# Kernel tuning notes

Measured on AMD Instinct MI355X. Metric: run time of the kernel, lower is better.

Reference implementation:

```python
import jax, jax.numpy as jnp
import numpy as np

H = 64  # hidden size
I = 300  # input size
NEG_SLOPE = 0.01  # LeakyReLU default


def _gru_scan(x_proj, W_hh, b_hh):
    """x_proj: [T, B, 3H] precomputed input projections (+ b_ih).
    Returns all hidden states [T, B, H] starting from h0 = 0."""
    B = x_proj.shape[1]
    h0 = jnp.zeros((B, H), dtype=x_proj.dtype)

    def step(h, xp):
        gh = h @ W_hh.T + b_hh  # [B, 3H]
        xr, xz, xn = jnp.split(xp, 3, axis=-1)
        hr, hz, hn = jnp.split(gh, 3, axis=-1)
        r = jax.nn.sigmoid(xr + hr)
        z = jax.nn.sigmoid(xz + hz)
        n = jnp.tanh(xn + r * hn)
        h_new = (1.0 - z) * n + z * h
        return h_new, h_new

    _, hs = jax.lax.scan(step, h0, x_proj)
    return hs  # [T, B, H]


def _forward(x, W_ih_f, W_hh_f, b_ih_f, b_hh_f, W_ih_b, W_hh_b, b_ih_b, b_hh_b,
             W1, b1, W2, b2):
    # x: [B, T, I]
    xt = jnp.swapaxes(x, 0, 1)  # [T, B, I]
    xp_f = jnp.einsum('tbi,gi->tbg', xt, W_ih_f) + b_ih_f  # [T, B, 3H]
    xp_b = jnp.einsum('tbi,gi->tbg', xt[::-1], W_ih_b) + b_ih_b

    hs_f = _gru_scan(xp_f, W_hh_f, b_hh_f)            # [T, B, H]
    hs_b = _gru_scan(xp_b, W_hh_b, b_hh_b)[::-1]      # [T, B, H] (realigned)

    out = jnp.concatenate([hs_f, hs_b], axis=-1)      # [T, B, 2H]
    x_first = out[0]    # [B, 2H]
    x_last = out[-1]    # [B, 2H]
    feat = jnp.concatenate([x_first, x_last], axis=1)  # [B, 4H]

    h1 = feat @ W1.T + b1
    h1 = jnp.where(h1 >= 0, h1, NEG_SLOPE * h1)  # LeakyReLU
    return h1 @ W2.T + b2  # [B, 1]


def setup_inputs() -> dict:
    key = jax.random.key(0)
    ks = jax.random.split(key, 16)
    B, T = 256, 512
    s_gru = 1.0 / np.sqrt(H)
    s1 = 1.0 / np.sqrt(256)
    s2 = 1.0 / np.sqrt(32)
    u = lambda k, shape, s: jax.random.uniform(k, shape, jnp.float32, -s, s)
    return {
        'x': jax.random.normal(ks[0], (B, T, I), dtype=jnp.float32),
        'W_ih_f': u(ks[1], (3 * H, I), s_gru),
        'W_hh_f': u(ks[2], (3 * H, H), s_gru),
        'b_ih_f': u(ks[3], (3 * H,), s_gru),
        'b_hh_f': u(ks[4], (3 * H,), s_gru),
        'W_ih_b': u(ks[5], (3 * H, I), s_gru),
        'W_hh_b': u(ks[6], (3 * H, H), s_gru),
        'b_ih_b': u(ks[7], (3 * H,), s_gru),
        'b_hh_b': u(ks[8], (3 * H,), s_gru),
        'W1': u(ks[9], (32, 4 * H), s1),
        'b1': u(ks[10], (32,), s1),
        'W2': u(ks[11], (1, 32), s2),
        'b2': u(ks[12], (1,), s2),
    }


def reference(x, W_ih_f, W_hh_f, b_ih_f, b_hh_f, W_ih_b, W_hh_b, b_ih_b, b_hh_b,
              W1, b1, W2, b2):
    return _forward(x, W_ih_f, W_hh_f, b_ih_f, b_hh_f,
                    W_ih_b, W_hh_b, b_ih_b, b_hh_b, W1, b1, W2, b2)
```

## Files before the change

### kernel.cpp

```cpp
#include <hip/hip_runtime.h>
#include <hip/hip_bf16.h>
#include <math.h>

#define T_LEN 512
#define B_SZ  256
#define I_SZ  300
#define H_SZ  64
#define G3    192
#define TPG   3072
#define HPAD  80

typedef float    f4v __attribute__((ext_vector_type(4)));
typedef _Float16 h4v __attribute__((ext_vector_type(4)));
typedef _Float16 h8v __attribute__((ext_vector_type(8)));

__device__ __forceinline__ float sigm_f(float x) {
    return __builtin_amdgcn_rcpf(1.f + __expf(-x));
}
__device__ __forceinline__ float tanh_f(float x) {
    float a = fabsf(x);
    float e = __expf(2.f * a);
    float t = 1.f - 2.f * __builtin_amdgcn_rcpf(1.f + e);
    return copysignf(t, x);
}

__device__ __forceinline__ void lds_barrier() {
    __builtin_amdgcn_sched_barrier(0);
    asm volatile("s_waitcnt lgkmcnt(0)\n\ts_barrier" ::: "memory");
    __builtin_amdgcn_sched_barrier(0);
}

#define KC  64
#define NKC 5

__device__ __forceinline__ int stage_off(int j, int srow, int skq) {
    int g2 = (skq >> 1) & 3;
    return j * 1024 + (skq >> 3) * 512 + g2 * 128 + ((srow ^ (g2 << 1)) << 3) + (skq & 1) * 4;
}
__device__ __forceinline__ int frag_off(int tile, int kh, int lane) {
    int kgrp = lane >> 4, fr = lane & 15;
    return tile * 1024 + kh * 512 + kgrp * 128 + (((fr ^ (kgrp << 1))) << 3);
}

__global__ __launch_bounds__(256, 2) void proj_gemm(
    const float* __restrict__ x,
    const float* __restrict__ Wf, const float* __restrict__ bf,
    const float* __restrict__ Wb, const float* __restrict__ bb,
    _Float16* __restrict__ xp)
{
    __shared__ _Float16 Ap[8 * 1024];
    __shared__ _Float16 Bp[12 * 1024];

    const int tid = threadIdx.x;
    const int bid = blockIdx.x;
    const int d   = bid >> 10;
    const int G   = (bid >> 6) & 15;
    const int tc  = bid & 63;

    const float* W    = d ? Wb : Wf;
    const float* bias = d ? bb : bf;

    const int srow = tid >> 4;
    const int skq  = tid & 15;

    const int lane = tid & 63;
    const int w    = tid >> 6;

    f4v acc[2][12];
    #pragma unroll
    for (int t2 = 0; t2 < 2; ++t2)
        #pragma unroll
        for (int gt = 0; gt < 12; ++gt) acc[t2][gt] = (f4v)0.f;

    float4 av[8], bv[12];
    {
        const bool valid = (skq * 4) <= 296;
        #pragma unroll
        for (int j = 0; j < 8; ++j)
            av[j] = valid ? *(const float4*)(x + ((size_t)(G * 16 + srow) * T_LEN + tc * 8 + j) * I_SZ + skq * 4)
                          : float4{0.f, 0.f, 0.f, 0.f};
        #pragma unroll
        for (int j = 0; j < 12; ++j)
            bv[j] = valid ? *(const float4*)(W + (size_t)(j * 16 + srow) * I_SZ + skq * 4)
                          : float4{0.f, 0.f, 0.f, 0.f};
    }

    for (int kc = 0; kc < NKC; ++kc) {
        __syncthreads();

        #pragma unroll
        for (int j = 0; j < 8; ++j) {
            h4v c = { (_Float16)av[j].x, (_Float16)av[j].y,
                      (_Float16)av[j].z, (_Float16)av[j].w };
            *(h4v*)&Ap[stage_off(j, srow, skq)] = c;
        }
        #pragma unroll
        for (int j = 0; j < 12; ++j) {
            h4v c = { (_Float16)bv[j].x, (_Float16)bv[j].y,
                      (_Float16)bv[j].z, (_Float16)bv[j].w };
            *(h4v*)&Bp[stage_off(j, srow, skq)] = c;
        }
        __syncthreads();

        if (kc + 1 < NKC) {
            const int k0 = (kc + 1) * KC;
            const bool valid = (k0 + skq * 4) <= 296;
            #pragma unroll
            for (int j = 0; j < 8; ++j)
                av[j] = valid ? *(const float4*)(x + ((size_t)(G * 16 + srow) * T_LEN + tc * 8 + j) * I_SZ + k0 + skq * 4)
                              : float4{0.f, 0.f, 0.f, 0.f};
            #pragma unroll
            for (int j = 0; j < 12; ++j)
                bv[j] = valid ? *(const float4*)(W + (size_t)(j * 16 + srow) * I_SZ + k0 + skq * 4)
                              : float4{0.f, 0.f, 0.f, 0.f};
        }

        #pragma unroll
        for (int kh = 0; kh < 2; ++kh) {
            h8v xb0 = *(const h8v*)&Ap[frag_off(w * 2 + 0, kh, lane)];
            h8v xb1 = *(const h8v*)&Ap[frag_off(w * 2 + 1, kh, lane)];
            #pragma unroll
            for (int gt = 0; gt < 12; ++gt) {
                h8v wf = *(const h8v*)&Bp[frag_off(gt, kh, lane)];
                acc[0][gt] = __builtin_amdgcn_mfma_f32_16x16x32_f16(wf, xb0, acc[0][gt], 0, 0, 0);
                acc[1][gt] = __builtin_amdgcn_mfma_f32_16x16x32_f16(wf, xb1, acc[1][gt], 0, 0, 0);
            }
        }
    }

    const int col  = lane & 15;
    const int rowq = lane >> 4;
    _Float16* obase = xp + (size_t)(d * 16 + G) * T_LEN * TPG;
    #pragma unroll
    for (int t2 = 0; t2 < 2; ++t2) {
        int t = tc * 8 + w * 2 + t2;
        _Float16* ot = obase + (size_t)t * TPG;
        #pragma unroll
        for (int gt = 0; gt < 12; ++gt) {
            float4 bv4 = *(const float4*)(bias + gt * 16 + rowq * 4);
            h4v c = { (_Float16)(acc[t2][gt][0] + bv4.x),
                      (_Float16)(acc[t2][gt][1] + bv4.y),
                      (_Float16)(acc[t2][gt][2] + bv4.z),
                      (_Float16)(acc[t2][gt][3] + bv4.w) };
            *(h4v*)(ot + col * G3 + gt * 16 + rowq * 4) = c;
        }
    }
}

__global__ __launch_bounds__(256) void gru_scan(
    const _Float16* __restrict__ xp2,
    const float* __restrict__ Whf, const float* __restrict__ bhf,
    const float* __restrict__ Whb, const float* __restrict__ bhb,
    float* __restrict__ feat)
{
    const int tid  = threadIdx.x;
    const int lane = tid & 63;
    const int w    = tid >> 6;
    const int blk  = blockIdx.x;
    const int d    = blk >> 6;
    const int G    = (blk >> 2) & 15;
    const int sub  = blk & 3;
    const int col  = lane & 15;
    const int quad = lane >> 4;
    const int u    = w * 16 + col;
    const int bm   = sub * 4 + quad;

    const float* Whh = d ? Whb : Whf;
    const float* bhh = d ? bhb : bhf;

    h8v wb[3][2];
    f4v accb[3];
    int loff[3];
    #pragma unroll
    for (int g = 0; g < 3; ++g) {
        const int n = g * 64 + u;
        const float* wrow = Whh + (size_t)n * 64;
        #pragma unroll
        for (int c = 0; c < 2; ++c) {
            float4 w0 = *(const float4*)(wrow + c * 32 + quad * 8);
            float4 w1 = *(const float4*)(wrow + c * 32 + quad * 8 + 4);
            wb[g][c] = h8v{(_Float16)w0.x, (_Float16)w0.y, (_Float16)w0.z, (_Float16)w0.w,
                           (_Float16)w1.x, (_Float16)w1.y, (_Float16)w1.z, (_Float16)w1.w};
        }
        float bn = bhh[n];
        accb[g] = f4v{bn, bn, bn, bn};
        loff[g] = bm * G3 + n;
    }

    __shared__ _Float16 hs[2][4 * HPAD];
    for (int i = tid; i < 4 * HPAD; i += 256) hs[0][i] = (_Float16)0.f;
    float hold = 0.f;

    const long tstep = d ? -(long)TPG : (long)TPG;
    const _Float16* base = xp2 + (size_t)(d * 16 + G) * T_LEN * TPG
                               + (size_t)(d ? T_LEN - 1 : 0) * TPG;

    _Float16 px[2][3];
    #pragma unroll
    for (int g = 0; g < 3; ++g) {
        px[0][g] = base[loff[g]];
        px[1][g] = base[tstep + loff[g]];
    }
    const _Float16* pnext = base + 2 * tstep;

    const int off_first = d ? 192 : 0;
    const int off_last  = d ? 64 : 128;

    __syncthreads();

    for (int s = 0; s < T_LEN; s += 2) {
        #pragma unroll
        for (int j = 0; j < 2; ++j) {
            const int sj = s + j;
            const _Float16* hrd = hs[j];
            _Float16*       hwr = hs[j ^ 1];

            h8v a0 = *(const h8v*)&hrd[(col >> 2) * HPAD + quad * 8];
            h8v a1 = *(const h8v*)&hrd[(col >> 2) * HPAD + 32 + quad * 8];

            f4v gh[3];
            #pragma unroll
            for (int g = 0; g < 3; ++g) {
                f4v t0 = __builtin_amdgcn_mfma_f32_16x16x32_f16(a0, wb[g][0], accb[g], 0, 0, 0);
                gh[g]  = __builtin_amdgcn_mfma_f32_16x16x32_f16(a1, wb[g][1], t0, 0, 0, 0);
            }

            _Float16 xc0 = px[j][0], xc1 = px[j][1], xc2 = px[j][2];
            if (sj + 2 < T_LEN) {
                #pragma unroll
                for (int g = 0; g < 3; ++g)
                    px[j][g] = pnext[loff[g]];
                pnext += tstep;
            }

            {
                float r = sigm_f((float)xc0 + gh[0][0]);
                float z = sigm_f((float)xc1 + gh[1][0]);
                float n = tanh_f((float)xc2 + r * gh[2][0]);
                float h = fmaf(z, hold - n, n);
                hold = h;
                hwr[quad * HPAD + u] = (_Float16)h;
            }

            if (sj == 0)
                feat[(G * 16 + bm) * 256 + off_first + u] = hold;
            if (sj == T_LEN - 1)
                feat[(G * 16 + bm) * 256 + off_last + u] = hold;

            lds_barrier();
        }
    }
}

__global__ __launch_bounds__(64) void head_k(
    const float* __restrict__ feat,
    const float* __restrict__ W1, const float* __restrict__ b1,
    const float* __restrict__ W2, const float* __restrict__ b2,
    float* __restrict__ out)
{
    __shared__ float fs[256];
    const int b = blockIdx.x;
    const int tid = threadIdx.x;
    *(float4*)&fs[tid * 4] = *(const float4*)&feat[b * 256 + tid * 4];
    __syncthreads();
    float v = 0.f;
    if (tid < 32) {
        float a = b1[tid];
        const float4* Wv = (const float4*)(W1 + tid * 256);
        const float4* fv = (const float4*)fs;
        #pragma unroll 8
        for (int k = 0; k < 64; ++k) {
            float4 wv = Wv[k], f = fv[k];
            a += wv.x * f.x + wv.y * f.y + wv.z * f.z + wv.w * f.w;
        }
        a = a >= 0.f ? a : 0.01f * a;
        v = a * W2[tid];
    }
    #pragma unroll
    for (int off = 16; off > 0; off >>= 1) v += __shfl_down(v, off);
    if (tid == 0) out[b] = v + b2[0];
}

extern "C" void kernel_launch(void* const* d_in, const int* in_sizes, int n_in,
                              void* d_out, int out_size, void* d_ws, size_t ws_size,
                              hipStream_t stream)
{
    const float* x    = (const float*)d_in[0];
    const float* Wihf = (const float*)d_in[1];
    const float* Whhf = (const float*)d_in[2];
    const float* bihf = (const float*)d_in[3];
    const float* bhhf = (const float*)d_in[4];
    const float* Wihb = (const float*)d_in[5];
    const float* Whhb = (const float*)d_in[6];
    const float* bihb = (const float*)d_in[7];
    const float* bhhb = (const float*)d_in[8];
    const float* W1   = (const float*)d_in[9];
    const float* b1   = (const float*)d_in[10];
    const float* W2   = (const float*)d_in[11];
    const float* b2   = (const float*)d_in[12];
    float* out = (float*)d_out;

    _Float16* xp2  = (_Float16*)d_ws;
    float*    feat = (float*)((char*)d_ws + (size_t)2 * B_SZ * T_LEN * G3 * 2);

    proj_gemm<<<2048, 256, 0, stream>>>(x, Wihf, bihf, Wihb, bihb, xp2);
    gru_scan<<<128, 256, 0, stream>>>(xp2, Whhf, bhhf, Whhb, bhhb, feat);
    head_k<<<256, 64, 0, stream>>>(feat, W1, b1, W2, b2, out);
}
```

Baseline: 550.7 us.

## Keep full W_ih in LDS and load x fragments directly into registers

The projection GEMM now stages the whole converted fp16 input weight matrix into LDS once per block, using 120 KB of LDS. Each block then loops over four time chunks with 512 threads, loading x straight from global memory into MFMA fragment registers with no LDS staging and no per-k-chunk barriers. Each block covers 64 timesteps instead of 8, and the grid drops from 2048 to 256 blocks. This removes the repeated weight reloads and syncs, but the large LDS footprint limits occupancy to one block per CU. The direct per-lane x loads may also coalesce poorly.

```diff
diff --git a/kernel.cpp b/kernel.cpp
--- a/kernel.cpp
+++ b/kernel.cpp
@@ -42,107 +42,101 @@
     return tile * 1024 + kh * 512 + kgrp * 128 + (((fr ^ (kgrp << 1))) << 3);
 }
 
-__global__ __launch_bounds__(256, 2) void proj_gemm(
+__global__ __launch_bounds__(512, 2) void proj_gemm(
     const float* __restrict__ x,
     const float* __restrict__ Wf, const float* __restrict__ bf,
     const float* __restrict__ Wb, const float* __restrict__ bb,
     _Float16* __restrict__ xp)
 {
-    __shared__ _Float16 Ap[8 * 1024];
-    __shared__ _Float16 Bp[12 * 1024];
+    __shared__ _Float16 Bp[NKC * 12 * 1024];
 
     const int tid = threadIdx.x;
     const int bid = blockIdx.x;
-    const int d   = bid >> 10;
-    const int G   = (bid >> 6) & 15;
-    const int tc  = bid & 63;
+    const int d   = bid >> 7;
+    const int G   = (bid >> 3) & 15;
+    const int tcc = bid & 7;
 
     const float* W    = d ? Wb : Wf;
     const float* bias = d ? bb : bf;
 
-    const int srow = tid >> 4;
-    const int skq  = tid & 15;
+    {
+        const int srow5 = tid >> 4;
+        const int skq   = tid & 15;
+        const int row   = srow5 & 15;
+        const int jW    = srow5 >> 4;
+        #pragma unroll
+        for (int kc = 0; kc < NKC; ++kc) {
+            const bool valid = (kc * KC + skq * 4) <= 296;
+            #pragma unroll
+            for (int jj = 0; jj < 6; ++jj) {
+                const int tile = jW * 6 + jj;
+                float4 v = valid ? *(const float4*)(W + (size_t)(tile * 16 + row) * I_SZ + kc * KC + skq * 4)
+                                 : float4{0.f, 0.f, 0.f, 0.f};
+                h4v c = { (_Float16)v.x, (_Float16)v.y, (_Float16)v.z, (_Float16)v.w };
+                *(h4v*)&Bp[kc * 12288 + stage_off(tile, row, skq)] = c;
+            }
+        }
+    }
+    __syncthreads();
 
     const int lane = tid & 63;
     const int w    = tid >> 6;
-
-    f4v acc[2][12];
-    #pragma unroll
-    for (int t2 = 0; t2 < 2; ++t2)
-        #pragma unroll
-        for (int gt = 0; gt < 12; ++gt) acc[t2][gt] = (f4v)0.f;
-
-    float4 av[8], bv[12];
-    {
-        const bool valid = (skq * 4) <= 296;
-        #pragma unroll
-        for (int j = 0; j < 8; ++j)
-            av[j] = valid ? *(const float4*)(x + ((size_t)(G * 16 + srow) * T_LEN + tc * 8 + j) * I_SZ + skq * 4)
-                          : float4{0.f, 0.f, 0.f, 0.f};
-        #pragma unroll
-        for (int j = 0; j < 12; ++j)
-            bv[j] = valid ? *(const float4*)(W + (size_t)(j * 16 + srow) * I_SZ + skq * 4)
-                          : float4{0.f, 0.f, 0.f, 0.f};
-    }
-
-    for (int kc = 0; kc < NKC; ++kc) {
-        __syncthreads();
-
-        #pragma unroll
-        for (int j = 0; j < 8; ++j) {
-            h4v c = { (_Float16)av[j].x, (_Float16)av[j].y,
-                      (_Float16)av[j].z, (_Float16)av[j].w };
-            *(h4v*)&Ap[stage_off(j, srow, skq)] = c;
-        }
-        #pragma unroll
-        for (int j = 0; j < 12; ++j) {
-            h4v c = { (_Float16)bv[j].x, (_Float16)bv[j].y,
-                      (_Float16)bv[j].z, (_Float16)bv[j].w };
-            *(h4v*)&Bp[stage_off(j, srow, skq)] = c;
-        }
-        __syncthreads();
-
-        if (kc + 1 < NKC) {
-            const int k0 = (kc + 1) * KC;
-            const bool valid = (k0 + skq * 4) <= 296;
-            #pragma unroll
-            for (int j = 0; j < 8; ++j)
-                av[j] = valid ? *(const float4*)(x + ((size_t)(G * 16 + srow) * T_LEN + tc * 8 + j) * I_SZ + k0 + skq * 4)
-                              : float4{0.f, 0.f, 0.f, 0.f};
-            #pragma unroll
-            for (int j = 0; j < 12; ++j)
-                bv[j] = valid ? *(const float4*)(W + (size_t)(j * 16 + srow) * I_SZ + k0 + skq * 4)
-                              : float4{0.f, 0.f, 0.f, 0.f};
-        }
-
-        #pragma unroll
-        for (int kh = 0; kh < 2; ++kh) {
-            h8v xb0 = *(const h8v*)&Ap[frag_off(w * 2 + 0, kh, lane)];
-            h8v xb1 = *(const h8v*)&Ap[frag_off(w * 2 + 1, kh, lane)];
-            #pragma unroll
-            for (int gt = 0; gt < 12; ++gt) {
-                h8v wf = *(const h8v*)&Bp[frag_off(gt, kh, lane)];
-                acc[0][gt] = __builtin_amdgcn_mfma_f32_16x16x32_f16(wf, xb0, acc[0][gt], 0, 0, 0);
-                acc[1][gt] = __builtin_amdgcn_mfma_f32_16x16x32_f16(wf, xb1, acc[1][gt], 0, 0, 0);
-            }
-        }
-    }
+    const int kgrp = lane >> 4;
+    const int fr   = lane & 15;
+
+    const float* xrow = x + (size_t)(G * 16 + fr) * T_LEN * I_SZ;
 
     const int col  = lane & 15;
     const int rowq = lane >> 4;
     _Float16* obase = xp + (size_t)(d * 16 + G) * T_LEN * TPG;
-    #pragma unroll
-    for (int t2 = 0; t2 < 2; ++t2) {
-        int t = tc * 8 + w * 2 + t2;
-        _Float16* ot = obase + (size_t)t * TPG;
-        #pragma unroll
-        for (int gt = 0; gt < 12; ++gt) {
-            float4 bv4 = *(const float4*)(bias + gt * 16 + rowq * 4);
-            h4v c = { (_Float16)(acc[t2][gt][0] + bv4.x),
-                      (_Float16)(acc[t2][gt][1] + bv4.y),
-                      (_Float16)(acc[t2][gt][2] + bv4.z),
-                      (_Float16)(acc[t2][gt][3] + bv4.w) };
-            *(h4v*)(ot + col * G3 + gt * 16 + rowq * 4) = c;
+
+    for (int tch = 0; tch < 4; ++tch) {
+        const int t0 = tcc * 64 + tch * 16 + w * 2;
+
+        f4v acc[2][12];
+        #pragma unroll
+        for (int t2 = 0; t2 < 2; ++t2)
+            #pragma unroll
+            for (int gt = 0; gt < 12; ++gt) acc[t2][gt] = (f4v)0.f;
+
+        #pragma unroll
+        for (int kc = 0; kc < NKC; ++kc) {
+            h8v xb[2][2];
+            #pragma unroll
+            for (int t2 = 0; t2 < 2; ++t2) {
+                const float* xt = xrow + (size_t)(t0 + t2) * I_SZ;
+                #pragma unroll
+                for (int kh = 0; kh < 2; ++kh) {
+                    const int k0 = kc * KC + kh * 32 + kgrp * 8;
+                    float4 lo = (k0     <= 296) ? *(const float4*)(xt + k0)     : float4{0.f,0.f,0.f,0.f};
+                    float4 hi = (k0 + 4 <= 296) ? *(const float4*)(xt + k0 + 4) : float4{0.f,0.f,0.f,0.f};
+                    xb[t2][kh] = h8v{(_Float16)lo.x,(_Float16)lo.y,(_Float16)lo.z,(_Float16)lo.w,
+                                     (_Float16)hi.x,(_Float16)hi.y,(_Float16)hi.z,(_Float16)hi.w};
+                }
+            }
+            #pragma unroll
+            for (int kh = 0; kh < 2; ++kh) {
+                #pragma unroll
+                for (int gt = 0; gt < 12; ++gt) {
+                    h8v wf = *(const h8v*)&Bp[kc * 12288 + frag_off(gt, kh, lane)];
+                    acc[0][gt] = __builtin_amdgcn_mfma_f32_16x16x32_f16(wf, xb[0][kh], acc[0][gt], 0, 0, 0);
+                    acc[1][gt] = __builtin_amdgcn_mfma_f32_16x16x32_f16(wf, xb[1][kh], acc[1][gt], 0, 0, 0);
+                }
+            }
+        }
+
+        #pragma unroll
+        for (int t2 = 0; t2 < 2; ++t2) {
+            _Float16* ot = obase + (size_t)(t0 + t2) * TPG;
+            #pragma unroll
+            for (int gt = 0; gt < 12; ++gt) {
+                float4 bv4 = *(const float4*)(bias + gt * 16 + rowq * 4);
+                h4v c = { (_Float16)(acc[t2][gt][0] + bv4.x),
+                          (_Float16)(acc[t2][gt][1] + bv4.y),
+                          (_Float16)(acc[t2][gt][2] + bv4.z),
+                          (_Float16)(acc[t2][gt][3] + bv4.w) };
+                *(h4v*)(ot + col * G3 + gt * 16 + rowq * 4) = c;
+            }
         }
     }
 }
@@ -303,7 +297,7 @@
     _Float16* xp2  = (_Float16*)d_ws;
     float*    feat = (float*)((char*)d_ws + (size_t)2 * B_SZ * T_LEN * G3 * 2);
 
-    proj_gemm<<<2048, 256, 0, stream>>>(x, Wihf, bihf, Wihb, bihb, xp2);
+    proj_gemm<<<256, 512, 0, stream>>>(x, Wihf, bihf, Wihb, bihb, xp2);
     gru_scan<<<128, 256, 0, stream>>>(xp2, Whhf, bhhf, Whhb, bhhb, feat);
     head_k<<<256, 64, 0, stream>>>(feat, W1, b1, W2, b2, out);
 }
```

Result: slower. 707.2 us (+28.4%).
